# Optimization experiments

Hardware: AMD Instinct MI355X
Metric: run time of the kernel (lower is better)

Reference implementation:

```python
import jax, jax.numpy as jnp
from jax import lax
import numpy as np

MAX_D = 4  # max_displacement


def conv3x3(x, w, b):
    # x: [B,Cin,H,W], w: [Cout,Cin,3,3], SAME padding (pad=1)
    y = lax.conv_general_dilated(
        x, w, window_strides=(1, 1), padding='SAME',
        dimension_numbers=('NCHW', 'OIHW', 'NCHW'))
    return y + b[None, :, None, None]


def compute_cost_volume(f1, f2, d):
    # roll+mask in the torch code == shift with zero padding:
    # cv[idx,h,w] = mean_c f1[c,h,w] * f2[c,h-i,w-j] (zero outside bounds)
    B, C, H, W = f1.shape
    pad = jnp.pad(f2, ((0, 0), (0, 0), (d, d), (d, d)))
    slices = []
    for i in range(-d, d + 1):
        for j in range(-d, d + 1):
            shifted = lax.dynamic_slice(pad, (0, 0, d - i, d - j), (B, C, H, W))
            slices.append((f1 * shifted).sum(axis=1) / C)  # [B,H,W]
    return jnp.stack(slices, axis=1)  # [B,81,H,W]


def setup_inputs() -> dict:
    key = jax.random.key(0)
    ks = jax.random.split(key, 10)
    B, C, H, W = 16, 64, 128, 128
    cv_ch = (2 * MAX_D + 1) ** 2  # 81
    def w_init(k, shape):
        fan_in = shape[1] * shape[2] * shape[3]
        return jax.random.normal(k, shape, dtype=jnp.float32) * np.float32(np.sqrt(2.0 / fan_in))
    return {
        'f1': jax.random.normal(ks[0], (B, C, H, W), dtype=jnp.float32),
        'f2_warped': jax.random.normal(ks[1], (B, C, H, W), dtype=jnp.float32),
        'w1': w_init(ks[2], (128, C + cv_ch, 3, 3)),
        'b1': jnp.zeros((128,), dtype=jnp.float32),
        'w2': w_init(ks[3], (64, 128, 3, 3)),
        'b2': jnp.zeros((64,), dtype=jnp.float32),
        'w3': w_init(ks[4], (32, 64, 3, 3)),
        'b3': jnp.zeros((32,), dtype=jnp.float32),
        'w4': w_init(ks[5], (2, 32, 3, 3)),
        'b4': jnp.zeros((2,), dtype=jnp.float32),
    }


def reference(f1, f2_warped, w1, b1, w2, b2, w3, b3, w4, b4):
    cv = compute_cost_volume(f1, f2_warped, MAX_D)       # [B,81,H,W]
    x = jnp.concatenate([f1, cv], axis=1)                # [B,145,H,W]
    x = jax.nn.relu(conv3x3(x, w1, b1))
    x = jax.nn.relu(conv3x3(x, w2, b2))
    x = jax.nn.relu(conv3x3(x, w3, b3))
    flow = conv3x3(x, w4, b4)                            # [B,2,H,W]
    return flow
```

## Files before the change

### kernel.cpp

```cpp
#include <hip/hip_runtime.h>


typedef __bf16 bf16x8 __attribute__((ext_vector_type(8)));
typedef float f32x4 __attribute__((ext_vector_type(4)));

__device__ __forceinline__ unsigned short f2bf_bits(float f) {
  unsigned int u = __float_as_uint(f);
  unsigned int r = (u + 0x7FFFu + ((u >> 16) & 1u)) >> 16;
  return (unsigned short)r;
}

__device__ __forceinline__ void glds16(const ushort* gp, ushort* lp) {
  __builtin_amdgcn_global_load_lds((const __attribute__((address_space(1))) void*)gp,
                                   (__attribute__((address_space(3))) void*)lp, 16, 0, 0);
}

__global__ __launch_bounds__(256) void prep_w_all_kernel(
    const float* __restrict__ w1, const float* __restrict__ w2,
    const float* __restrict__ w3, const float* __restrict__ w4,
    uint4* __restrict__ wp1, uint4* __restrict__ wp2,
    uint4* __restrict__ wp3, uint4* __restrict__ wp4) {
  const int bx = blockIdx.x;
  const float* w; uint4* wp; int CIN, COUT, CHUNKS, NFRAG, base;
  if (bx < 90)       { w = w1; wp = wp1; CIN = 145; COUT = 128; CHUNKS = 5; NFRAG = 8; base = 0; }
  else if (bx < 126) { w = w2; wp = wp2; CIN = 128; COUT = 64;  CHUNKS = 4; NFRAG = 4; base = 90; }
  else if (bx < 135) { w = w3; wp = wp3; CIN = 64;  COUT = 32;  CHUNKS = 2; NFRAG = 2; base = 126; }
  else               { w = w4; wp = wp4; CIN = 32;  COUT = 2;   CHUNKS = 1; NFRAG = 1; base = 135; }
  int idx = (bx - base) * 256 + threadIdx.x;
  int total = CHUNKS * 9 * NFRAG * 64;
  if (idx >= total) return;
  int lane = idx & 63;
  int fi = idx >> 6;
  int nf = fi % NFRAG;
  int t = fi / NFRAG;
  int rs = t % 9;
  int c = t / 9;
  int co = nf * 16 + (lane & 15);
  int cib = c * 32 + (lane >> 4) * 8;
  union { uint4 q; ushort s[8]; } pk;
#pragma unroll
  for (int e = 0; e < 8; ++e) {
    int ci = cib + e;
    float v = (ci < CIN && co < COUT) ? w[(co * CIN + ci) * 9 + rs] : 0.f;
    pk.s[e] = f2bf_bits(v);
  }
  wp[idx] = pk.q;
}

__global__ __launch_bounds__(256) void pack_both_kernel(const float* __restrict__ f1,
                                                        const float* __restrict__ f2,
                                                        ushort* __restrict__ xf1,
                                                        ushort* __restrict__ xf2) {
  __shared__ float tile[64][132];
  const int bid0 = blockIdx.x;
  const float* src = (bid0 < 2048) ? f1 : f2;
  ushort* dst = (bid0 < 2048) ? xf1 : xf2;
  const int bid = bid0 & 2047;
  const int h = bid & 127, b = bid >> 7;
  const int tid = threadIdx.x;
  for (int e = tid; e < 64 * 128; e += 256) {
    int c = e >> 7, w = e & 127;
    tile[c][w] = src[((b * 64 + c) * 128 + h) * 128 + w];
  }
  __syncthreads();
  const int px = tid >> 1, cgb = (tid & 1) * 4;
  const long base = ((long)(b * 128 + h) * 128 + px) * 64;
#pragma unroll
  for (int e = 0; e < 4; ++e) {
    int c0 = (cgb + e) * 8;
    union { uint4 q; ushort s[8]; } pk;
#pragma unroll
    for (int k = 0; k < 8; ++k) pk.s[k] = f2bf_bits(tile[c0 + k][px]);
    *reinterpret_cast<uint4*>(&dst[base + c0]) = pk.q;
  }
}

__global__ __launch_bounds__(256)
void cost_volume_mfma_kernel(const ushort* __restrict__ xf1,
                             const ushort* __restrict__ xf2,
                             ushort* __restrict__ xcv) {
  const int bx = blockIdx.x;
  const int idx = bx >> 3;
  const int b = 2 * (bx & 7) + (idx >> 7);
  const int h = idx & 127;
  const int tid = threadIdx.x;
  const int lane = tid & 63;
  const int g = tid >> 6;
  const int l15 = lane & 15;
  const int lg = lane >> 4;

  __shared__ __align__(16) float sC[4][2][16][33];
  __shared__ __align__(16) ushort sO[96][132];

  {
    uint4 z = make_uint4(0u, 0u, 0u, 0u);
    uint4* p = (uint4*)sO;
#pragma unroll
    for (int j = 0; j < 7; ++j) {
      int e = tid + j * 256;
      if (e < 1584) p[e] = z;
    }
  }
  __syncthreads();

  const int w0g = g * 32;
  bf16x8 afr[2][2];
  {
    const ushort* f1p = xf1 + ((long)(b * 128 + h) * 128) * 64;
#pragma unroll
    for (int wt = 0; wt < 2; ++wt)
#pragma unroll
      for (int kc = 0; kc < 2; ++kc) {
        int pix = w0g + wt * 16 + l15;
        afr[wt][kc] = *reinterpret_cast<const bf16x8*>(f1p + pix * 64 + kc * 32 + lg * 8);
      }
  }

  const float inv = 1.0f / 64.0f;
  for (int A = 0; A < 9; ++A) {
    int fr = h - 4 + A;
    if ((unsigned)fr >= 128u) continue;
    const ushort* f2p = xf2 + ((long)(b * 128 + fr) * 128) * 64;
    bf16x8 bfr[3][2];
#pragma unroll
    for (int t = 0; t < 3; ++t)
#pragma unroll
      for (int kc = 0; kc < 2; ++kc) {
        int p = w0g - 4 + t * 16 + l15;
        uint4 v = make_uint4(0u, 0u, 0u, 0u);
        if ((unsigned)p < 128u)
          v = *reinterpret_cast<const uint4*>(f2p + (long)p * 64 + kc * 32 + lg * 8);
        bfr[t][kc] = __builtin_bit_cast(bf16x8, v);
      }
#pragma unroll
    for (int wt = 0; wt < 2; ++wt)
#pragma unroll
      for (int nt = 0; nt < 2; ++nt) {
        f32x4 acc = {0.f, 0.f, 0.f, 0.f};
        acc = __builtin_amdgcn_mfma_f32_16x16x32_bf16(afr[wt][0], bfr[wt + nt][0], acc, 0, 0, 0);
        acc = __builtin_amdgcn_mfma_f32_16x16x32_bf16(afr[wt][1], bfr[wt + nt][1], acc, 0, 0, 0);
#pragma unroll
        for (int j = 0; j < 4; ++j)
          sC[g][wt][lg * 4 + j][nt * 16 + l15] = acc[j];
      }
    const int chb = (8 - A) * 9;
#pragma unroll
    for (int wt = 0; wt < 2; ++wt) {
      int px = w0g + wt * 16 + l15;
#pragma unroll
      for (int u = 0; u < 3; ++u) {
        if (u < ((lg == 3) ? 3 : 2)) {
          int tj = lg * 2 + u;
          float v = sC[g][wt][l15][l15 + 8 - tj];
          sO[chb + tj][px] = f2bf_bits(v * inv);
        }
      }
    }
  }
  __syncthreads();

  uint4* dst = reinterpret_cast<uint4*>(xcv + ((long)(b * 128 + h) * 128) * 96);
#pragma unroll
  for (int j = 0; j < 6; ++j) {
    int t8 = j * 256 + tid;
    int px = t8 / 12;
    int ch0 = (t8 - px * 12) * 8;
    union { uint4 qq; ushort ss[8]; } pk;
#pragma unroll
    for (int k = 0; k < 8; ++k) pk.ss[k] = sO[ch0 + k][px];
    dst[t8] = pk.qq;
  }
}

template <int CA, int CB, int COUT, bool RELU, bool PLANAR>
__global__ __launch_bounds__(512, 2)
void conv_mfma_kernel(const ushort* __restrict__ xa, const ushort* __restrict__ xb,
                      const uint4* __restrict__ wp, const float* __restrict__ bias,
                      void* __restrict__ outv) {
  constexpr int CHUNKS = (CA + CB) / 32;
  constexpr int NFRAG = COUT / 16;
  constexpr int NFW = (NFRAG >= 2) ? NFRAG / 2 : 1;
  constexpr int MFW = (NFRAG >= 2) ? 4 : 2;
  constexpr int SXN = 4 * 130 * 32;
  constexpr int WTQ = 9 * NFRAG * 64;
  constexpr int WTA_Q = 5 * NFRAG * 64;
  constexpr int WTB_Q = 4 * NFRAG * 64;
  constexpr int WIA = (WTA_Q + 511) / 512;
  constexpr int WIB = (WTB_Q + 511) / 512;
  constexpr int SO_STRIDE = COUT + 4;
  constexpr int STAGE_B = PLANAR ? 2048 : 2 * 128 * SO_STRIDE * 2;
  constexpr int SX_B = 2 * SXN * 2;
  constexpr int BASE_B = SX_B + (WTA_Q + WTB_Q) * 16;
  constexpr int ARENA_B = STAGE_B > BASE_B ? STAGE_B : BASE_B;

  __shared__ __align__(16) char arena[ARENA_B];
  ushort* sXa = (ushort*)arena;
  ushort* sWtA = (ushort*)(arena + SX_B);
  ushort* sWtB = (ushort*)(arena + SX_B + WTA_Q * 16);

  const int bx = blockIdx.x;
  const int idx = bx >> 3;
  const int b = 2 * (bx & 7) + (idx >> 6);
  const int h0 = (idx & 63) * 2;
  const int tid = threadIdx.x;
  const int lane = tid & 63;
  const int wid = tid >> 6;
  const int l15 = lane & 15;
  const int lg = lane >> 4;
  const int cg    = (NFRAG >= 2) ? (wid >> 2) : 0;
  const int row   = (NFRAG >= 2) ? ((wid >> 1) & 1) : (wid >> 2);
  const int pbase = (NFRAG >= 2) ? ((wid & 1) * 64) : ((wid & 3) * 32);
  const bool act_wave = ((unsigned)(h0 - 1 + (wid >> 1)) < 128u);

  f32x4 acc[MFW][NFW];
#pragma unroll
  for (int mf = 0; mf < MFW; ++mf)
#pragma unroll
    for (int nf = 0; nf < NFW; ++nf) acc[mf][nf] = {0.f, 0.f, 0.f, 0.f};

  if (tid < 64) {
    int bi = tid >> 5, tr = (tid >> 3) & 3, wz = (tid >> 2) & 1, gq = tid & 3;
    int wl = wz ? 129 : 0;
    *reinterpret_cast<uint4*>(&sXa[bi * SXN + ((tr * 130 + wl) * 4 + gq) * 8]) =
        make_uint4(0u, 0u, 0u, 0u);
  }
  if (h0 == 0 || h0 == 126) {
    const int trz = (h0 == 0) ? 0 : 3;
#pragma unroll
    for (int e = 0; e < 2; ++e) {
      int u = tid + e * 512;
      int bi = u >> 9, k = u & 511;
      *reinterpret_cast<uint4*>(&sXa[bi * SXN + ((trz * 130 + 1) * 4 + k) * 8]) =
          make_uint4(0u, 0u, 0u, 0u);
    }
  }

  auto stage = [&](int c, int bi) {
    const int c0 = c * 32;
    const ushort* src;
    int cst, coff;
    if (CB == 0 || c0 < CA) { src = xa; cst = CA; coff = c0; }
    else                    { src = xb; cst = CB; coff = c0 - CA; }
    const int tr = wid >> 1;
    const int gh = h0 - 1 + tr;
    if ((unsigned)gh < 128u) {
      const ushort* rowp = src + ((long)(b * 128 + gh) * 128) * cst + coff;
#pragma unroll
      for (int t = 0; t < 4; ++t) {
        int s = (wid & 1) * 4 + t;
        int u = s * 64 + lane;
        int wl = 1 + (u >> 2);
        int gq = lane & 3;
        int sw = (wl + (wl >> 2)) & 3;
        const ushort* gp = rowp + (long)(wl - 1) * cst + (gq ^ sw) * 8;
        ushort* lp = &sXa[bi * SXN + ((tr * 130 + 1) * 4 + s * 64) * 8];
        glds16(gp, lp);
      }
    }
  };

  auto stage_wtA = [&](int c) {
    const ushort* src = (const ushort*)(wp + (size_t)c * WTQ);
#pragma unroll
    for (int i = 0; i < WIA; ++i) {
      int e = tid + i * 512;
      if ((WTA_Q % 512) == 0 || e < WTA_Q)
        glds16(src + (size_t)e * 8, sWtA + (size_t)(tid & ~63) * 8 + (size_t)(i * 512) * 8);
    }
  };
  auto stage_wtB = [&](int c) {
    const ushort* src = (const ushort*)(wp + (size_t)c * WTQ + WTA_Q);
#pragma unroll
    for (int i = 0; i < WIB; ++i) {
      int e = tid + i * 512;
      if ((WTB_Q % 512) == 0 || e < WTB_Q)
        glds16(src + (size_t)e * 8, sWtB + (size_t)(tid & ~63) * 8 + (size_t)(i * 512) * 8);
    }
  };

  auto compute = [&](int bi, int rs0, int rs1, const ushort* wbuf) {
#pragma unroll
    for (int rs = rs0; rs < rs1; ++rs) {
      const int r = rs / 3, s = rs % 3;
      const int tr = row + r;
      bf16x8 afr[MFW];
#pragma unroll
      for (int mf = 0; mf < MFW; ++mf) {
        int wl = pbase + mf * 16 + l15 + s;
        int sw = (wl + (wl >> 2)) & 3;
        afr[mf] = *reinterpret_cast<const bf16x8*>(
            &sXa[bi * SXN + ((tr * 130 + wl) * 4 + (lg ^ sw)) * 8]);
      }
      const ushort* wrow = wbuf + (size_t)((rs - rs0) * NFRAG + cg * NFW) * 64 * 8;
#pragma unroll
      for (int nf = 0; nf < NFW; ++nf) {
        bf16x8 bfr = *reinterpret_cast<const bf16x8*>(wrow + (nf * 64 + lane) * 8);
#pragma unroll
        for (int mf = 0; mf < MFW; ++mf)
          acc[mf][nf] = __builtin_amdgcn_mfma_f32_16x16x32_bf16(afr[mf], bfr, acc[mf][nf], 0, 0, 0);
      }
    }
  };

  stage(0, 0);
  stage_wtA(0);
  __syncthreads();

  for (int c = 0; c < CHUNKS; ++c) {
    const int bi = c & 1;
    stage_wtB(c);
    const bool act_issued = (c + 1 < CHUNKS) && act_wave;
    if (c + 1 < CHUNKS) stage(c + 1, bi ^ 1);
    compute(bi, 0, 5, sWtA);
    if (act_issued) asm volatile("s_waitcnt vmcnt(4)" ::: "memory");
    else            asm volatile("s_waitcnt vmcnt(0)" ::: "memory");
    __builtin_amdgcn_s_barrier();
    asm volatile("" ::: "memory");
    if (c + 1 < CHUNKS) stage_wtA(c + 1);
    compute(bi, 5, 9, sWtB);
    asm volatile("s_waitcnt vmcnt(0)" ::: "memory");
    __builtin_amdgcn_s_barrier();
    asm volatile("" ::: "memory");
  }

  if (!PLANAR) {
    ushort* sO = (ushort*)arena;
#pragma unroll
    for (int nf = 0; nf < NFW; ++nf) {
      float bs = bias[cg * NFW * 16 + nf * 16 + l15];
#pragma unroll
      for (int mf = 0; mf < MFW; ++mf) {
        int px2 = row * 128 + pbase + mf * 16 + lg * 4;
#pragma unroll
        for (int j = 0; j < 4; ++j) {
          float v = acc[mf][nf][j] + bs;
          if (RELU) v = fmaxf(v, 0.f);
          sO[(px2 + j) * SO_STRIDE + cg * NFW * 16 + nf * 16 + l15] = f2bf_bits(v);
        }
      }
    }
    __syncthreads();
    constexpr int QPP = COUT / 8;
    uint4* dst = reinterpret_cast<uint4*>((ushort*)outv + ((long)(b * 128 + h0) * 128) * COUT);
#pragma unroll
    for (int t0 = 0; t0 < 2 * 128 * QPP / 512; ++t0) {
      int t = t0 * 512 + tid;
      int px2 = t / QPP;
      int ch0 = (t & (QPP - 1)) * 8;
      union { uint4 qq; ushort ss[8]; } pk;
#pragma unroll
      for (int k = 0; k < 8; ++k) pk.ss[k] = sO[px2 * SO_STRIDE + ch0 + k];
      dst[t] = pk.qq;
    }
  } else {
    float* sF = (float*)arena;
    if (l15 < 2) {
#pragma unroll
      for (int mf = 0; mf < MFW; ++mf) {
        int pxb = pbase + mf * 16 + lg * 4;
#pragma unroll
        for (int j = 0; j < 4; ++j)
          sF[(l15 * 2 + row) * 128 + pxb + j] = acc[mf][0][j] + bias[l15];
      }
    }
    __syncthreads();
    float* out = (float*)outv;
    if (tid < 128) {
      int ch = tid >> 6, r = (tid >> 5) & 1, qx = tid & 31;
      *reinterpret_cast<float4*>(&out[((long)(b * 2 + ch) * 128 + h0 + r) * 128 + qx * 4]) =
          *reinterpret_cast<float4*>(&sF[(ch * 2 + r) * 128 + qx * 4]);
    }
  }
}

extern "C" void kernel_launch(void* const* d_in, const int* in_sizes, int n_in,
                              void* d_out, int out_size, void* d_ws, size_t ws_size,
                              hipStream_t stream) {
  (void)in_sizes; (void)n_in; (void)out_size; (void)ws_size;
  const float* f1 = (const float*)d_in[0];
  const float* f2 = (const float*)d_in[1];
  const float* w1 = (const float*)d_in[2];
  const float* b1 = (const float*)d_in[3];
  const float* w2 = (const float*)d_in[4];
  const float* b2 = (const float*)d_in[5];
  const float* w3 = (const float*)d_in[6];
  const float* b3 = (const float*)d_in[7];
  const float* w4 = (const float*)d_in[8];
  const float* b4 = (const float*)d_in[9];

  char* ws = (char*)d_ws;
  size_t off = 0;
  ushort* xf1 = (ushort*)(ws + off); off += (size_t)262144 * 64 * 2;
  ushort* xcv = (ushort*)(ws + off); off += (size_t)262144 * 96 * 2;
  ushort* x1  = (ushort*)(ws + off); off += (size_t)262144 * 128 * 2;
  ushort* x2  = (ushort*)(ws + off); off += (size_t)262144 * 64 * 2;
  uint4* wp1 = (uint4*)(ws + off); off += (size_t)5 * 9 * 8 * 64 * 16;
  uint4* wp2 = (uint4*)(ws + off); off += (size_t)4 * 9 * 4 * 64 * 16;
  uint4* wp3 = (uint4*)(ws + off); off += (size_t)2 * 9 * 2 * 64 * 16;
  uint4* wp4 = (uint4*)(ws + off); off += (size_t)1 * 9 * 1 * 64 * 16;
  ushort* x3  = xf1;
  ushort* xf2 = x1;

  prep_w_all_kernel<<<138, 256, 0, stream>>>(w1, w2, w3, w4, wp1, wp2, wp3, wp4);
  pack_both_kernel<<<4096, 256, 0, stream>>>(f1, f2, xf1, xf2);
  cost_volume_mfma_kernel<<<2048, 256, 0, stream>>>(xf1, xf2, xcv);

  conv_mfma_kernel<64, 96, 128, true, false><<<1024, 512, 0, stream>>>(xf1, xcv, wp1, b1, x1);
  conv_mfma_kernel<128, 0, 64, true, false><<<1024, 512, 0, stream>>>(x1, x1, wp2, b2, x2);
  conv_mfma_kernel<64, 0, 32, true, false><<<1024, 512, 0, stream>>>(x2, x2, wp3, b3, x3);
  conv_mfma_kernel<32, 0, 16, false, true><<<1024, 512, 0, stream>>>(x3, x3, wp4, b4, d_out);
}
```

Measured before the change: 289.4 us.

## Add 1024-thread four-row conv kernel for first two layers with per-kh-row weight staging

Adds a new conv kernel in which each 1024-thread block computes four output rows instead of two. This halves the redundant halo-row activation loads per block and raises weight reuse per staged fragment. Weights are staged one kernel row at a time (3 taps) in a double buffer, with a barrier after each row. The old kernel's fine-grained vmcnt waits are replaced by plain __syncthreads. The larger block and larger LDS footprint may lower occupancy and add synchronisation points.

```diff
diff --git a/kernel.cpp b/kernel.cpp
--- a/kernel.cpp
+++ b/kernel.cpp
@@ -172,6 +172,172 @@
   }
 }
 
+template <int CA, int CB, int COUT, bool RELU>
+__global__ __launch_bounds__(1024, 4)
+void conv_mfma16_kernel(const ushort* __restrict__ xa, const ushort* __restrict__ xb,
+                        const uint4* __restrict__ wp, const float* __restrict__ bias,
+                        ushort* __restrict__ out) {
+  constexpr int CHUNKS = (CA + CB) / 32;
+  constexpr int NFRAG = COUT / 16;
+  constexpr int CGDIV = (COUT == 128) ? 2 : 1;
+  constexpr int NFW = NFRAG / CGDIV;
+  constexpr int MFW = (CGDIV == 2) ? 4 : 2;
+  constexpr int MH = 128 / (MFW * 16);
+  constexpr int SXN = 6 * 130 * 32;
+  constexpr int SX_B = 2 * SXN * 2;
+  constexpr int WPQ = 3 * NFRAG * 64;
+  constexpr int NSEG = WPQ / 64;
+  constexpr int SO_STRIDE = COUT + 4;
+  constexpr int SO_B = 512 * SO_STRIDE * 2;
+  constexpr int BASE_B = SX_B + 2 * WPQ * 16;
+  constexpr int ARENA_B = (SO_B > BASE_B) ? SO_B : BASE_B;
+
+  __shared__ __align__(16) char arena[ARENA_B];
+  ushort* sXa = (ushort*)arena;
+  uint4* sWt = (uint4*)(arena + SX_B);
+
+  const int bx = blockIdx.x;
+  const int idx = bx >> 3;
+  const int b = 2 * (bx & 7) + (idx >> 5);
+  const int h0 = (idx & 31) * 4;
+  const int tid = threadIdx.x;
+  const int lane = tid & 63;
+  const int wid = tid >> 6;
+  const int l15 = lane & 15, lg = lane >> 4;
+  const int cg = (CGDIV == 2) ? (wid >> 3) : 0;
+  const int wrem = (CGDIV == 2) ? (wid & 7) : wid;
+  const int row = (MH == 2) ? (wrem >> 1) : (wrem >> 2);
+  const int mh = wrem & (MH - 1);
+  const int pbase = mh * (MFW * 16);
+
+  f32x4 acc[MFW][NFW];
+#pragma unroll
+  for (int mf = 0; mf < MFW; ++mf)
+#pragma unroll
+    for (int nf = 0; nf < NFW; ++nf) acc[mf][nf] = {0.f, 0.f, 0.f, 0.f};
+
+  if (tid < 96) {
+    int bi = tid / 48, rem = tid % 48;
+    int tr = rem >> 3, wz = (rem >> 2) & 1, g = rem & 3;
+    int wl = wz ? 129 : 0;
+    *reinterpret_cast<uint4*>(&sXa[bi * SXN + ((tr * 130 + wl) * 4 + g) * 8]) =
+        make_uint4(0u, 0u, 0u, 0u);
+  }
+  if (h0 == 0 || h0 == 124) {
+    int trz = (h0 == 0) ? 0 : 5;
+    for (int e = tid; e < 1040; e += 1024) {
+      int bi = e / 520, k = e % 520;
+      *reinterpret_cast<uint4*>(&sXa[bi * SXN + (trz * 520 + k) * 8]) =
+          make_uint4(0u, 0u, 0u, 0u);
+    }
+  }
+
+  auto stage_act = [&](int c, int bi) {
+    const int c0 = c * 32;
+    const ushort* src; int cst, coff;
+    if (CB == 0 || c0 < CA) { src = xa; cst = CA; coff = c0; }
+    else                    { src = xb; cst = CB; coff = c0 - CA; }
+#pragma unroll
+    for (int i = 0; i < 3; ++i) {
+      int sidx = wid + i * 16;
+      int tr = sidx >> 3, seg = sidx & 7;
+      int gh = h0 - 1 + tr;
+      if ((unsigned)gh < 128u) {
+        const ushort* rowp = src + ((long)(b * 128 + gh) * 128) * cst + coff;
+        int u = seg * 64 + lane;
+        int wl = 1 + (u >> 2);
+        int g = lane & 3;
+        int sw = (wl + (wl >> 2)) & 3;
+        const ushort* gp = rowp + (long)(wl - 1) * cst + (g ^ sw) * 8;
+        ushort* lp = &sXa[bi * SXN + ((tr * 130 + 1) * 4 + seg * 64) * 8];
+        glds16(gp, lp);
+      }
+    }
+  };
+
+  auto stage_wt = [&](int c, int p, int bs) {
+    const ushort* src = (const ushort*)(wp + (size_t)(c * 9 + p * 3) * NFRAG * 64);
+#pragma unroll
+    for (int i = 0; i < 2; ++i) {
+      int sidx = wid + i * 16;
+      if (sidx < NSEG) {
+        ushort* lp = (ushort*)(sWt + bs * WPQ + sidx * 64);
+        glds16(src + (size_t)(sidx * 64 + lane) * 8, lp);
+      }
+    }
+  };
+
+  auto compute = [&](int p, int bs, int bi) {
+    const int tr = row + p;
+#pragma unroll
+    for (int s = 0; s < 3; ++s) {
+      bf16x8 afr[MFW];
+#pragma unroll
+      for (int mf = 0; mf < MFW; ++mf) {
+        int wl = pbase + mf * 16 + l15 + s;
+        int sw = (wl + (wl >> 2)) & 3;
+        afr[mf] = *reinterpret_cast<const bf16x8*>(
+            &sXa[bi * SXN + ((tr * 130 + wl) * 4 + (lg ^ sw)) * 8]);
+      }
+#pragma unroll
+      for (int nf = 0; nf < NFW; ++nf) {
+        bf16x8 bfr = __builtin_bit_cast(bf16x8,
+            sWt[bs * WPQ + (s * NFRAG + cg * NFW + nf) * 64 + lane]);
+#pragma unroll
+        for (int mf = 0; mf < MFW; ++mf)
+          acc[mf][nf] = __builtin_amdgcn_mfma_f32_16x16x32_bf16(afr[mf], bfr, acc[mf][nf], 0, 0, 0);
+      }
+    }
+  };
+
+  stage_act(0, 0);
+  stage_wt(0, 0, 0);
+  __syncthreads();
+
+  for (int c = 0; c < CHUNKS; ++c) {
+    const int bi = c & 1;
+    if (c + 1 < CHUNKS) stage_act(c + 1, bi ^ 1);
+    stage_wt(c, 1, (3 * c + 1) & 1);
+    compute(0, (3 * c) & 1, bi);
+    __syncthreads();
+    stage_wt(c, 2, (3 * c + 2) & 1);
+    compute(1, (3 * c + 1) & 1, bi);
+    __syncthreads();
+    if (c + 1 < CHUNKS) stage_wt(c + 1, 0, (3 * c + 3) & 1);
+    compute(2, (3 * c + 2) & 1, bi);
+    __syncthreads();
+  }
+
+  ushort* sO = (ushort*)arena;
+#pragma unroll
+  for (int nf = 0; nf < NFW; ++nf) {
+    float bs = bias[cg * NFW * 16 + nf * 16 + l15];
+#pragma unroll
+    for (int mf = 0; mf < MFW; ++mf) {
+      int px2 = row * 128 + pbase + mf * 16 + lg * 4;
+#pragma unroll
+      for (int j = 0; j < 4; ++j) {
+        float v = acc[mf][nf][j] + bs;
+        if (RELU) v = fmaxf(v, 0.f);
+        sO[(px2 + j) * SO_STRIDE + cg * NFW * 16 + nf * 16 + l15] = f2bf_bits(v);
+      }
+    }
+  }
+  __syncthreads();
+  constexpr int QPP = COUT / 8;
+  uint4* dst = reinterpret_cast<uint4*>(out + ((long)(b * 128 + h0) * 128) * COUT);
+#pragma unroll
+  for (int t0 = 0; t0 < 512 * QPP / 1024; ++t0) {
+    int t = t0 * 1024 + tid;
+    int px2 = t / QPP;
+    int ch0 = (t & (QPP - 1)) * 8;
+    union { uint4 qq; ushort ss[8]; } pk;
+#pragma unroll
+    for (int k = 0; k < 8; ++k) pk.ss[k] = sO[px2 * SO_STRIDE + ch0 + k];
+    dst[t] = pk.qq;
+  }
+}
+
 template <int CA, int CB, int COUT, bool RELU, bool PLANAR>
 __global__ __launch_bounds__(512, 2)
 void conv_mfma_kernel(const ushort* __restrict__ xa, const ushort* __restrict__ xb,
@@ -210,7 +376,6 @@
   const int cg    = (NFRAG >= 2) ? (wid >> 2) : 0;
   const int row   = (NFRAG >= 2) ? ((wid >> 1) & 1) : (wid >> 2);
   const int pbase = (NFRAG >= 2) ? ((wid & 1) * 64) : ((wid & 3) * 32);
-  const bool act_wave = ((unsigned)(h0 - 1 + (wid >> 1)) < 128u);
 
   f32x4 acc[MFW][NFW];
 #pragma unroll
@@ -309,18 +474,12 @@
   for (int c = 0; c < CHUNKS; ++c) {
     const int bi = c & 1;
     stage_wtB(c);
-    const bool act_issued = (c + 1 < CHUNKS) && act_wave;
     if (c + 1 < CHUNKS) stage(c + 1, bi ^ 1);
     compute(bi, 0, 5, sWtA);
-    if (act_issued) asm volatile("s_waitcnt vmcnt(4)" ::: "memory");
-    else            asm volatile("s_waitcnt vmcnt(0)" ::: "memory");
-    __builtin_amdgcn_s_barrier();
-    asm volatile("" ::: "memory");
+    __syncthreads();
     if (c + 1 < CHUNKS) stage_wtA(c + 1);
     compute(bi, 5, 9, sWtB);
-    asm volatile("s_waitcnt vmcnt(0)" ::: "memory");
-    __builtin_amdgcn_s_barrier();
-    asm volatile("" ::: "memory");
+    __syncthreads();
   }
 
   if (!PLANAR) {
@@ -405,8 +564,8 @@
   pack_both_kernel<<<4096, 256, 0, stream>>>(f1, f2, xf1, xf2);
   cost_volume_mfma_kernel<<<2048, 256, 0, stream>>>(xf1, xf2, xcv);
 
-  conv_mfma_kernel<64, 96, 128, true, false><<<1024, 512, 0, stream>>>(xf1, xcv, wp1, b1, x1);
-  conv_mfma_kernel<128, 0, 64, true, false><<<1024, 512, 0, stream>>>(x1, x1, wp2, b2, x2);
+  conv_mfma16_kernel<64, 96, 128, true><<<512, 1024, 0, stream>>>(xf1, xcv, wp1, b1, x1);
+  conv_mfma16_kernel<128, 0, 64, true><<<512, 1024, 0, stream>>>(x1, x1, wp2, b2, x2);
   conv_mfma_kernel<64, 0, 32, true, false><<<1024, 512, 0, stream>>>(x2, x2, wp3, b3, x3);
   conv_mfma_kernel<32, 0, 16, false, true><<<1024, 512, 0, stream>>>(x3, x3, wp4, b4, d_out);
 }
```

After: 432.3 us. 1.49x slower.
